# Optimization experiments

Hardware: AMD Instinct MI355X
Metric: run time of the kernel (lower is better)

## Reference

```python
import jax, jax.numpy as jnp
import numpy as np

# Faithful math of the torch module (dropout in eval mode => identity):
#   alpha = sigmoid(smoothing_weight)                       # [h,1] -> [1,1,h,1]
#   out[t] = alpha^(t+1) * v0 + sum_{s<=t} (1-alpha) alpha^(t-s) * values[s]
#   aux path kernel: weight/clamp(1-alpha,1e-6)*alpha => factor*alpha^(t-s+1)
#     with factor = (1-alpha)/max(1-alpha,1e-6) (== 1 unless alpha ~ 1)
# The torch code realizes this causal linear recurrence via FFT cross-correlation;
# here we use an associative (parallel) scan, which computes the same sums.

B, T, H, D = 8, 4096, 8, 64

def setup_inputs() -> dict:
    key = jax.random.key(0)
    k1, k2, k3, k4 = jax.random.split(key, 4)
    values = jax.random.normal(k1, (B, T, H, D), dtype=jnp.float32)
    aux_values = jax.random.normal(k2, (B, T, H, D), dtype=jnp.float32)
    v0 = jax.random.normal(k3, (1, 1, H, D), dtype=jnp.float32)
    smoothing_weight = jax.random.normal(k4, (H, 1), dtype=jnp.float32)
    return {"values": values, "aux_values": aux_values, "v0": v0,
            "smoothing_weight": smoothing_weight}

def reference(values, aux_values, v0, smoothing_weight):
    b, t, h, d = values.shape
    alpha = jax.nn.sigmoid(smoothing_weight).reshape(1, 1, h, 1)  # [1,1,h,1]
    one_m = 1.0 - alpha
    factor = one_m / jnp.maximum(one_m, 1e-6)  # == 1 unless alpha ~ 1 (clamp in torch)
    # Linear recurrence y[t] = alpha*y[t-1] + u[t], y[-1] = v0, where
    # u[t] = (1-alpha)*values[t] + factor*alpha*aux_values[t] (fused main + aux path).
    a = jnp.broadcast_to(alpha, (1, t, h, 1))               # decay coeffs
    u = one_m * values + (factor * alpha) * aux_values      # [b,t,h,d]
    def combine(c1, c2):
        a1, b1 = c1
        a2, b2 = c2
        return (a1 * a2, a2 * b1 + b2)
    A, Bsum = jax.lax.associative_scan(combine, (a, u), axis=1)
    # A[t] = alpha^(t+1); Bsum[t] = sum_{s<=t} alpha^(t-s) * u[s]
    return A * v0 + Bsum
```

## Files before the change

### kernel.cpp

```cpp
#include <hip/hip_runtime.h>
#include <math.h>

#define BB 8
#define TT 4096
#define HH 8
#define DD 64

typedef float f32x4_native __attribute__((ext_vector_type(4)));

__device__ __forceinline__ float sigmoidf_(float x) {
    return 1.0f / (1.0f + expf(-x));
}

template<int NCv>
__global__ __launch_bounds__(128)
void k_agg(const float4* __restrict__ vals, const float4* __restrict__ aux,
           const float* __restrict__ w, float4* __restrict__ Z) {
    constexpr int L = TT / NCv;
    const int blk = blockIdx.x;
    const int b = blk / NCv, c = blk % NCv;
    const int tid = threadIdx.x;
    const int h = tid >> 4;

    const float alpha = sigmoidf_(w[h]);
    const float onem  = 1.0f - alpha;
    const float fa    = (onem / fmaxf(onem, 1e-6f)) * alpha;

    int base = (b * TT + c * L) * 128 + tid;

    float4 y = make_float4(0.f, 0.f, 0.f, 0.f);
#pragma unroll
    for (int hh = 0; hh < L / 8; ++hh) {
        float4 v[8], a[8];
#pragma unroll
        for (int i = 0; i < 8; ++i) {
            v[i] = vals[base + (hh * 8 + i) * 128];
            a[i] = aux [base + (hh * 8 + i) * 128];
        }
#pragma unroll
        for (int i = 0; i < 8; ++i) {
            y.x = alpha * y.x + (onem * v[i].x + fa * a[i].x);
            y.y = alpha * y.y + (onem * v[i].y + fa * a[i].y);
            y.z = alpha * y.z + (onem * v[i].z + fa * a[i].z);
            y.w = alpha * y.w + (onem * v[i].w + fa * a[i].w);
        }
    }
    Z[(b * NCv + c) * 128 + tid] = y;
}

template<int NCv>
__global__ __launch_bounds__(512)
void k_scan(const float4* __restrict__ Z, const float* __restrict__ v0,
            const float* __restrict__ w, float4* __restrict__ P) {
    constexpr int L = TT / NCv;
    __shared__ float lds[NCv][9];

    const int blk = blockIdx.x;
    const int b  = blk >> 6;
    const int h  = (blk >> 3) & 7;
    const int d8 = blk & 7;
    const int r4 = h * 16 + d8 * 2;
    const int tid = threadIdx.x;

    const float alpha = sigmoidf_(w[h]);
    const float aL = powf(alpha, (float)L);

#pragma unroll
    for (int it = 0; it < 2; ++it) {
        int idx = it * NCv + tid;
        int c = idx >> 1, k = idx & 1;
        float4 z = Z[(b * NCv + c) * 128 + r4 + k];
        lds[c][k * 4 + 0] = z.x;
        lds[c][k * 4 + 1] = z.y;
        lds[c][k * 4 + 2] = z.z;
        lds[c][k * 4 + 3] = z.w;
    }
    __syncthreads();

    const int c = tid;
    float s[8];
#pragma unroll
    for (int k = 0; k < 8; ++k) s[k] = lds[c][k];

    float m = aL;
    for (int off = 1; off < NCv; off <<= 1) {
        float tmp[8];
        const bool act = (c >= off);
        if (act) {
#pragma unroll
            for (int k = 0; k < 8; ++k) tmp[k] = lds[c - off][k];
        }
        __syncthreads();
        if (act) {
#pragma unroll
            for (int k = 0; k < 8; ++k) { s[k] += m * tmp[k]; lds[c][k] = s[k]; }
        }
        m *= m;
        __syncthreads();
    }

    const float pc = powf(alpha, (float)(L * c));
    const float4* v04 = (const float4*)v0;
#pragma unroll
    for (int k = 0; k < 2; ++k) {
        float4 vv = v04[r4 + k];
        float4 pr;
        if (c == 0) {
            pr = vv;
        } else {
            pr.x = pc * vv.x + lds[c - 1][k * 4 + 0];
            pr.y = pc * vv.y + lds[c - 1][k * 4 + 1];
            pr.z = pc * vv.z + lds[c - 1][k * 4 + 2];
            pr.w = pc * vv.w + lds[c - 1][k * 4 + 3];
        }
        P[(b * NCv + c) * 128 + r4 + k] = pr;
    }
}

template<int NCv>
__global__ __launch_bounds__(128)
void k_out(const float4* __restrict__ vals, const float4* __restrict__ aux,
           const float* __restrict__ w, const float4* __restrict__ P,
           float4* __restrict__ out) {
    constexpr int L = TT / NCv;
    const int blk = blockIdx.x;
    const int b = blk / NCv, c = blk % NCv;
    const int tid = threadIdx.x;
    const int h = tid >> 4;

    const float alpha = sigmoidf_(w[h]);
    const float onem  = 1.0f - alpha;
    const float fa    = (onem / fmaxf(onem, 1e-6f)) * alpha;

    const float4 p = P[(b * NCv + c) * 128 + tid];
    int base = (b * TT + c * L) * 128 + tid;

    float4 y = make_float4(0.f, 0.f, 0.f, 0.f);
    float coef = alpha;
#pragma unroll
    for (int hh = 0; hh < L / 8; ++hh) {
        float4 v[8], a[8];
#pragma unroll
        for (int i = 0; i < 8; ++i) {
            v[i] = vals[base + (hh * 8 + i) * 128];
            a[i] = aux [base + (hh * 8 + i) * 128];
        }
#pragma unroll
        for (int i = 0; i < 8; ++i) {
            y.x = alpha * y.x + (onem * v[i].x + fa * a[i].x);
            y.y = alpha * y.y + (onem * v[i].y + fa * a[i].y);
            y.z = alpha * y.z + (onem * v[i].z + fa * a[i].z);
            y.w = alpha * y.w + (onem * v[i].w + fa * a[i].w);
            float4 o;
            o.x = y.x + coef * p.x;
            o.y = y.y + coef * p.y;
            o.z = y.z + coef * p.z;
            o.w = y.w + coef * p.w;
            __builtin_nontemporal_store(*(const f32x4_native*)&o,
                                        (f32x4_native*)&out[base + (hh * 8 + i) * 128]);
            coef *= alpha;
        }
    }
}

extern "C" void kernel_launch(void* const* d_in, const int* in_sizes, int n_in,
                              void* d_out, int out_size, void* d_ws, size_t ws_size,
                              hipStream_t stream) {
    const float4* vals = (const float4*)d_in[0];
    const float4* aux  = (const float4*)d_in[1];
    const float*  v0   = (const float*)d_in[2];
    const float*  w    = (const float*)d_in[3];

    float4* out = (float4*)d_out;

    const size_t need512 = 2ull * BB * 512 * 128 * sizeof(float4);

    if (ws_size >= need512) {
        constexpr int NCv = 512;
        float4* Z = (float4*)d_ws;
        float4* P = Z + (size_t)BB * NCv * 128;
        k_agg <NCv><<<BB * NCv,   128, 0, stream>>>(vals, aux, w, Z);
        k_scan<NCv><<<BB * HH * 8, NCv, 0, stream>>>(Z, v0, w, P);
        k_out <NCv><<<BB * NCv,   128, 0, stream>>>(vals, aux, w, P, out);
    } else {
        constexpr int NCv = 256;
        float4* Z = (float4*)d_ws;
        float4* P = Z + (size_t)BB * NCv * 128;
        k_agg <NCv><<<BB * NCv,   128, 0, stream>>>(vals, aux, w, Z);
        k_scan<NCv><<<BB * HH * 8, NCv, 0, stream>>>(Z, v0, w, P);
        k_out <NCv><<<BB * NCv,   128, 0, stream>>>(vals, aux, w, P, out);
    }
}
```

Measured before the change: 198.1 us.

## Fuse agg, scan and output into one persistent kernel with grid barriers

Replaces the three-kernel chunked scan with one kernel launched as a co-resident grid. Each block keeps its 16-step local prefix in registers, publishes chunk totals, hits a software grid barrier, and a subset of blocks runs the cross-chunk scan (two chunks per thread). After a second barrier every block applies the carry to its register-held results. The aim is to avoid reading values/aux a second time and to drop two launch gaps, at the cost of spin-barrier latency, a memset and an occupancy query per call. It relies on all 2048 blocks being resident at once, which is checked via the occupancy API (assumed 256 CUs); the old three-kernel path is kept as the fallback.

```diff
diff --git a/kernel.cpp b/kernel.cpp
--- a/kernel.cpp
+++ b/kernel.cpp
@@ -4,86 +4,202 @@
 #define BB 8
 #define TT 4096
 #define HH 8
-#define DD 64
-
-typedef float f32x4_native __attribute__((ext_vector_type(4)));
+#define NCC 256
+#define LC 16
+#define GRID (BB * NCC)
+
+typedef float f32x4 __attribute__((ext_vector_type(4)));
 
 __device__ __forceinline__ float sigmoidf_(float x) {
     return 1.0f / (1.0f + expf(-x));
 }
 
-template<int NCv>
+__device__ __forceinline__ void gbar(unsigned int* cnt, unsigned int* gen) {
+    __threadfence();
+    __syncthreads();
+    if (threadIdx.x == 0) {
+        unsigned int g = __hip_atomic_load(gen, __ATOMIC_RELAXED, __HIP_MEMORY_SCOPE_AGENT);
+        unsigned int old = __hip_atomic_fetch_add(cnt, 1u, __ATOMIC_ACQ_REL, __HIP_MEMORY_SCOPE_AGENT);
+        if (old == (unsigned int)(GRID - 1)) {
+            __hip_atomic_store(cnt, 0u, __ATOMIC_RELAXED, __HIP_MEMORY_SCOPE_AGENT);
+            __hip_atomic_store(gen, g + 1u, __ATOMIC_RELEASE, __HIP_MEMORY_SCOPE_AGENT);
+        } else {
+            while (__hip_atomic_load(gen, __ATOMIC_ACQUIRE, __HIP_MEMORY_SCOPE_AGENT) == g)
+                __builtin_amdgcn_s_sleep(8);
+        }
+    }
+    __syncthreads();
+    __threadfence();
+}
+
+__global__ __launch_bounds__(128, 4)
+void k_fused(const float4* __restrict__ vals, const float4* __restrict__ aux,
+             const float* __restrict__ v0, const float* __restrict__ w,
+             float4* __restrict__ Z, float4* __restrict__ P,
+             unsigned int* __restrict__ bar, float4* __restrict__ out) {
+    __shared__ float lds[128][9];
+
+    const int blk = blockIdx.x;
+    const int b = blk >> 8;
+    const int c = blk & (NCC - 1);
+    const int tid = threadIdx.x;
+    const int h = tid >> 4;
+
+    const float alpha = sigmoidf_(w[h]);
+    const float onem  = 1.0f - alpha;
+    const float fa    = (onem / fmaxf(onem, 1e-6f)) * alpha;
+
+    const int base = (b * TT + c * LC) * 128 + tid;
+
+    float4 y[LC];
+    {
+        float4 yy = make_float4(0.f, 0.f, 0.f, 0.f);
+#pragma unroll
+        for (int i = 0; i < LC; ++i) {
+            float4 v = vals[base + i * 128];
+            float4 a = aux[base + i * 128];
+            yy.x = alpha * yy.x + onem * v.x + fa * a.x;
+            yy.y = alpha * yy.y + onem * v.y + fa * a.y;
+            yy.z = alpha * yy.z + onem * v.z + fa * a.z;
+            yy.w = alpha * yy.w + onem * v.w + fa * a.w;
+            y[i] = yy;
+        }
+        Z[(b * NCC + c) * 128 + tid] = yy;
+    }
+
+    gbar(bar, bar + 1);
+
+    if (blk < BB * HH * 8) {
+        const int sb = blk >> 6;
+        const int sh = (blk >> 3) & 7;
+        const int d8 = blk & 7;
+        const int r4 = sh * 16 + d8 * 2;
+        const float sa  = sigmoidf_(w[sh]);
+        const float aL  = powf(sa, (float)LC);
+        const float aL2 = aL * aL;
+        const int t = tid;
+
+        float z0[8], s[8];
+        {
+            float4 za = Z[(sb * NCC + 2 * t) * 128 + r4];
+            float4 zb = Z[(sb * NCC + 2 * t) * 128 + r4 + 1];
+            float4 zc = Z[(sb * NCC + 2 * t + 1) * 128 + r4];
+            float4 zd = Z[(sb * NCC + 2 * t + 1) * 128 + r4 + 1];
+            z0[0]=za.x; z0[1]=za.y; z0[2]=za.z; z0[3]=za.w;
+            z0[4]=zb.x; z0[5]=zb.y; z0[6]=zb.z; z0[7]=zb.w;
+            float z1[8] = {zc.x,zc.y,zc.z,zc.w,zd.x,zd.y,zd.z,zd.w};
+#pragma unroll
+            for (int k = 0; k < 8; ++k) { s[k] = z1[k] + aL * z0[k]; lds[t][k] = s[k]; }
+        }
+        __syncthreads();
+
+        float m = aL2;
+        for (int off = 1; off < 128; off <<= 1) {
+            float tmp[8];
+            const bool act = (t >= off);
+            if (act) {
+#pragma unroll
+                for (int k = 0; k < 8; ++k) tmp[k] = lds[t - off][k];
+            }
+            __syncthreads();
+            if (act) {
+#pragma unroll
+                for (int k = 0; k < 8; ++k) { s[k] += m * tmp[k]; lds[t][k] = s[k]; }
+            }
+            m *= m;
+            __syncthreads();
+        }
+
+        float stm1[8];
+#pragma unroll
+        for (int k = 0; k < 8; ++k) stm1[k] = (t > 0) ? lds[t - 1][k] : 0.f;
+
+        const float pc0 = powf(sa, (float)(LC * 2 * t));
+        const float pc1 = pc0 * aL;
+        const float* v0p = v0 + sh * 64 + d8 * 8;
+        float4* Pp = P + (sb * NCC + 2 * t) * 128 + r4;
+        float p0[8], p1[8];
+#pragma unroll
+        for (int k = 0; k < 8; ++k) {
+            float vv  = v0p[k];
+            float s2t = z0[k] + aL * stm1[k];
+            p0[k] = pc0 * vv + stm1[k];
+            p1[k] = pc1 * vv + s2t;
+        }
+        float4 q;
+        q.x=p0[0]; q.y=p0[1]; q.z=p0[2]; q.w=p0[3]; Pp[0]   = q;
+        q.x=p0[4]; q.y=p0[5]; q.z=p0[6]; q.w=p0[7]; Pp[1]   = q;
+        q.x=p1[0]; q.y=p1[1]; q.z=p1[2]; q.w=p1[3]; Pp[128] = q;
+        q.x=p1[4]; q.y=p1[5]; q.z=p1[6]; q.w=p1[7]; Pp[129] = q;
+    }
+
+    gbar(bar, bar + 1);
+
+    const float4 p = P[(b * NCC + c) * 128 + tid];
+    float coef = alpha;
+#pragma unroll
+    for (int i = 0; i < LC; ++i) {
+        float4 o;
+        o.x = y[i].x + coef * p.x;
+        o.y = y[i].y + coef * p.y;
+        o.z = y[i].z + coef * p.z;
+        o.w = y[i].w + coef * p.w;
+        __builtin_nontemporal_store(*(const f32x4*)&o, (f32x4*)&out[base + i * 128]);
+        coef *= alpha;
+    }
+}
+
 __global__ __launch_bounds__(128)
 void k_agg(const float4* __restrict__ vals, const float4* __restrict__ aux,
            const float* __restrict__ w, float4* __restrict__ Z) {
-    constexpr int L = TT / NCv;
-    const int blk = blockIdx.x;
-    const int b = blk / NCv, c = blk % NCv;
+    const int blk = blockIdx.x;
+    const int b = blk >> 8, c = blk & (NCC - 1);
     const int tid = threadIdx.x;
     const int h = tid >> 4;
-
     const float alpha = sigmoidf_(w[h]);
     const float onem  = 1.0f - alpha;
     const float fa    = (onem / fmaxf(onem, 1e-6f)) * alpha;
-
-    int base = (b * TT + c * L) * 128 + tid;
-
-    float4 y = make_float4(0.f, 0.f, 0.f, 0.f);
-#pragma unroll
-    for (int hh = 0; hh < L / 8; ++hh) {
-        float4 v[8], a[8];
-#pragma unroll
-        for (int i = 0; i < 8; ++i) {
-            v[i] = vals[base + (hh * 8 + i) * 128];
-            a[i] = aux [base + (hh * 8 + i) * 128];
-        }
-#pragma unroll
-        for (int i = 0; i < 8; ++i) {
-            y.x = alpha * y.x + (onem * v[i].x + fa * a[i].x);
-            y.y = alpha * y.y + (onem * v[i].y + fa * a[i].y);
-            y.z = alpha * y.z + (onem * v[i].z + fa * a[i].z);
-            y.w = alpha * y.w + (onem * v[i].w + fa * a[i].w);
-        }
-    }
-    Z[(b * NCv + c) * 128 + tid] = y;
-}
-
-template<int NCv>
-__global__ __launch_bounds__(512)
+    const int base = (b * TT + c * LC) * 128 + tid;
+    float4 yy = make_float4(0.f, 0.f, 0.f, 0.f);
+#pragma unroll
+    for (int i = 0; i < LC; ++i) {
+        float4 v = vals[base + i * 128];
+        float4 a = aux[base + i * 128];
+        yy.x = alpha * yy.x + onem * v.x + fa * a.x;
+        yy.y = alpha * yy.y + onem * v.y + fa * a.y;
+        yy.z = alpha * yy.z + onem * v.z + fa * a.z;
+        yy.w = alpha * yy.w + onem * v.w + fa * a.w;
+    }
+    Z[(b * NCC + c) * 128 + tid] = yy;
+}
+
+__global__ __launch_bounds__(256)
 void k_scan(const float4* __restrict__ Z, const float* __restrict__ v0,
             const float* __restrict__ w, float4* __restrict__ P) {
-    constexpr int L = TT / NCv;
-    __shared__ float lds[NCv][9];
-
+    __shared__ float lds[NCC][9];
     const int blk = blockIdx.x;
     const int b  = blk >> 6;
     const int h  = (blk >> 3) & 7;
     const int d8 = blk & 7;
     const int r4 = h * 16 + d8 * 2;
     const int tid = threadIdx.x;
-
-    const float alpha = sigmoidf_(w[h]);
-    const float aL = powf(alpha, (float)L);
-
+    const float alpha = sigmoidf_(w[h]);
+    const float aL = powf(alpha, (float)LC);
 #pragma unroll
     for (int it = 0; it < 2; ++it) {
-        int idx = it * NCv + tid;
-        int c = idx >> 1, k = idx & 1;
-        float4 z = Z[(b * NCv + c) * 128 + r4 + k];
-        lds[c][k * 4 + 0] = z.x;
-        lds[c][k * 4 + 1] = z.y;
-        lds[c][k * 4 + 2] = z.z;
-        lds[c][k * 4 + 3] = z.w;
+        int idx = it * NCC + tid;
+        int cc = idx >> 1, k = idx & 1;
+        float4 z = Z[(b * NCC + cc) * 128 + r4 + k];
+        lds[cc][k * 4 + 0] = z.x; lds[cc][k * 4 + 1] = z.y;
+        lds[cc][k * 4 + 2] = z.z; lds[cc][k * 4 + 3] = z.w;
     }
     __syncthreads();
-
     const int c = tid;
     float s[8];
 #pragma unroll
     for (int k = 0; k < 8; ++k) s[k] = lds[c][k];
-
     float m = aL;
-    for (int off = 1; off < NCv; off <<= 1) {
+    for (int off = 1; off < NCC; off <<= 1) {
         float tmp[8];
         const bool act = (c >= off);
         if (act) {
@@ -98,8 +214,7 @@
         m *= m;
         __syncthreads();
     }
-
-    const float pc = powf(alpha, (float)(L * c));
+    const float pc = powf(alpha, (float)(LC * c));
     const float4* v04 = (const float4*)v0;
 #pragma unroll
     for (int k = 0; k < 2; ++k) {
@@ -113,53 +228,40 @@
             pr.z = pc * vv.z + lds[c - 1][k * 4 + 2];
             pr.w = pc * vv.w + lds[c - 1][k * 4 + 3];
         }
-        P[(b * NCv + c) * 128 + r4 + k] = pr;
-    }
-}
-
-template<int NCv>
+        P[(b * NCC + c) * 128 + r4 + k] = pr;
+    }
+}
+
 __global__ __launch_bounds__(128)
 void k_out(const float4* __restrict__ vals, const float4* __restrict__ aux,
            const float* __restrict__ w, const float4* __restrict__ P,
            float4* __restrict__ out) {
-    constexpr int L = TT / NCv;
-    const int blk = blockIdx.x;
-    const int b = blk / NCv, c = blk % NCv;
+    const int blk = blockIdx.x;
+    const int b = blk >> 8, c = blk & (NCC - 1);
     const int tid = threadIdx.x;
     const int h = tid >> 4;
-
     const float alpha = sigmoidf_(w[h]);
     const float onem  = 1.0f - alpha;
     const float fa    = (onem / fmaxf(onem, 1e-6f)) * alpha;
-
-    const float4 p = P[(b * NCv + c) * 128 + tid];
-    int base = (b * TT + c * L) * 128 + tid;
-
-    float4 y = make_float4(0.f, 0.f, 0.f, 0.f);
+    const float4 p = P[(b * NCC + c) * 128 + tid];
+    const int base = (b * TT + c * LC) * 128 + tid;
+    float4 yy = make_float4(0.f, 0.f, 0.f, 0.f);
     float coef = alpha;
 #pragma unroll
-    for (int hh = 0; hh < L / 8; ++hh) {
-        float4 v[8], a[8];
-#pragma unroll
-        for (int i = 0; i < 8; ++i) {
-            v[i] = vals[base + (hh * 8 + i) * 128];
-            a[i] = aux [base + (hh * 8 + i) * 128];
-        }
-#pragma unroll
-        for (int i = 0; i < 8; ++i) {
-            y.x = alpha * y.x + (onem * v[i].x + fa * a[i].x);
-            y.y = alpha * y.y + (onem * v[i].y + fa * a[i].y);
-            y.z = alpha * y.z + (onem * v[i].z + fa * a[i].z);
-            y.w = alpha * y.w + (onem * v[i].w + fa * a[i].w);
-            float4 o;
-            o.x = y.x + coef * p.x;
-            o.y = y.y + coef * p.y;
-            o.z = y.z + coef * p.z;
-            o.w = y.w + coef * p.w;
-            __builtin_nontemporal_store(*(const f32x4_native*)&o,
-                                        (f32x4_native*)&out[base + (hh * 8 + i) * 128]);
-            coef *= alpha;
-        }
+    for (int i = 0; i < LC; ++i) {
+        float4 v = vals[base + i * 128];
+        float4 a = aux[base + i * 128];
+        yy.x = alpha * yy.x + onem * v.x + fa * a.x;
+        yy.y = alpha * yy.y + onem * v.y + fa * a.y;
+        yy.z = alpha * yy.z + onem * v.z + fa * a.z;
+        yy.w = alpha * yy.w + onem * v.w + fa * a.w;
+        float4 o;
+        o.x = yy.x + coef * p.x;
+        o.y = yy.y + coef * p.y;
+        o.z = yy.z + coef * p.z;
+        o.w = yy.w + coef * p.w;
+        __builtin_nontemporal_store(*(const f32x4*)&o, (f32x4*)&out[base + i * 128]);
+        coef *= alpha;
     }
 }
 
@@ -170,24 +272,22 @@
     const float4* aux  = (const float4*)d_in[1];
     const float*  v0   = (const float*)d_in[2];
     const float*  w    = (const float*)d_in[3];
-
     float4* out = (float4*)d_out;
 
-    const size_t need512 = 2ull * BB * 512 * 128 * sizeof(float4);
-
-    if (ws_size >= need512) {
-        constexpr int NCv = 512;
-        float4* Z = (float4*)d_ws;
-        float4* P = Z + (size_t)BB * NCv * 128;
-        k_agg <NCv><<<BB * NCv,   128, 0, stream>>>(vals, aux, w, Z);
-        k_scan<NCv><<<BB * HH * 8, NCv, 0, stream>>>(Z, v0, w, P);
-        k_out <NCv><<<BB * NCv,   128, 0, stream>>>(vals, aux, w, P, out);
+    float4* Z = (float4*)d_ws;
+    float4* P = Z + (size_t)BB * NCC * 128;
+    unsigned int* bar = (unsigned int*)((char*)d_ws + 2ull * BB * NCC * 128 * sizeof(float4));
+
+    int nb = 0;
+    hipError_t e = hipOccupancyMaxActiveBlocksPerMultiprocessor(&nb, k_fused, 128, 0);
+    bool coop_ok = (e == hipSuccess) && ((long)nb * 256 >= GRID);
+
+    if (coop_ok) {
+        hipMemsetAsync(bar, 0, 16, stream);
+        k_fused<<<GRID, 128, 0, stream>>>(vals, aux, v0, w, Z, P, bar, out);
     } else {
-        constexpr int NCv = 256;
-        float4* Z = (float4*)d_ws;
-        float4* P = Z + (size_t)BB * NCv * 128;
-        k_agg <NCv><<<BB * NCv,   128, 0, stream>>>(vals, aux, w, Z);
-        k_scan<NCv><<<BB * HH * 8, NCv, 0, stream>>>(Z, v0, w, P);
-        k_out <NCv><<<BB * NCv,   128, 0, stream>>>(vals, aux, w, P, out);
-    }
-}
+        k_agg <<<GRID, 128, 0, stream>>>(vals, aux, w, Z);
+        k_scan<<<BB * HH * 8, NCC, 0, stream>>>(Z, v0, w, P);
+        k_out <<<GRID, 128, 0, stream>>>(vals, aux, w, P, out);
+    }
+}
```

New measurement: 198.1 us. Within noise of the previous version (-0.0%).
